# Kernel tuning notes

Measured on AMD Instinct MI355X. Metric: run time of the kernel, lower is better.

## Reference

```python
import jax, jax.numpy as jnp
import numpy as np
import math

D_MODEL = 768
H = 12
D_K = D_MODEL // H


def setup_inputs() -> dict:
    key = jax.random.key(0)
    ks = jax.random.split(key, 12)
    B, S = 2, 2048
    q = jax.random.normal(ks[0], (B, S, D_MODEL), dtype=jnp.float32)
    k = jax.random.normal(ks[1], (B, S, D_MODEL), dtype=jnp.float32)
    v = jax.random.normal(ks[2], (B, S, D_MODEL), dtype=jnp.float32)
    mask = jax.random.randint(ks[3], (1, 1, S, S), 0, 2, dtype=jnp.int32)
    scale = 1.0 / math.sqrt(D_MODEL)
    w_q = jax.random.normal(ks[4], (D_MODEL, D_MODEL), dtype=jnp.float32) * scale
    b_q = jnp.zeros((D_MODEL,), dtype=jnp.float32)
    w_k = jax.random.normal(ks[5], (D_MODEL, D_MODEL), dtype=jnp.float32) * scale
    b_k = jnp.zeros((D_MODEL,), dtype=jnp.float32)
    w_v = jax.random.normal(ks[6], (D_MODEL, D_MODEL), dtype=jnp.float32) * scale
    b_v = jnp.zeros((D_MODEL,), dtype=jnp.float32)
    w_o = jax.random.normal(ks[7], (D_MODEL, D_MODEL), dtype=jnp.float32) * scale
    b_o = jnp.zeros((D_MODEL,), dtype=jnp.float32)
    return {"q": q, "k": k, "v": v, "mask": mask,
            "w_q": w_q, "b_q": b_q, "w_k": w_k, "b_k": b_k,
            "w_v": w_v, "b_v": b_v, "w_o": w_o, "b_o": b_o}


def reference(q, k, v, mask, w_q, b_q, w_k, b_k, w_v, b_v, w_o, b_o):
    B, S, _ = q.shape
    # torch nn.Linear: y = x @ W^T + b
    qp = (q @ w_q.T + b_q).reshape(B, S, H, D_K).transpose(0, 2, 1, 3)  # [B,H,S,Dk]
    kp = (k @ w_k.T + b_k).reshape(B, S, H, D_K).transpose(0, 2, 1, 3)
    vp = (v @ w_v.T + b_v).reshape(B, S, H, D_K).transpose(0, 2, 1, 3)
    # full [B,H,S,S] score matrix (the memory-bound round-trip)
    scores = jnp.einsum('bhqd,bhkd->bhqk', qp, kp) / math.sqrt(D_K)
    scores = jnp.where(mask == 0, jnp.float32(-1e9), scores)
    attn = jax.nn.softmax(scores, axis=-1)
    x = jnp.einsum('bhqk,bhkd->bhqd', attn, vp)  # [B,H,S,Dk]
    x = x.transpose(0, 2, 1, 3).reshape(B, S, H * D_K)
    return x @ w_o.T + b_o
```

## Files before the change

kernel.cpp:

```cpp
#include <hip/hip_runtime.h>
#include <hip/hip_bf16.h>

typedef __attribute__((ext_vector_type(8))) __bf16 bf16x8;
typedef __attribute__((ext_vector_type(8))) short short8;
typedef __attribute__((ext_vector_type(4))) float f32x4;

#define LOG2E 1.44269504088896f
#define SCL (0.125f * 1.44269504088896f)

static __device__ __forceinline__ ushort f2bf(float f) {
  union { float f; unsigned u; } x; x.f = f;
  unsigned r = x.u + 0x7fffu + ((x.u >> 16) & 1u);
  return (ushort)(r >> 16);
}

static __device__ __forceinline__ unsigned cvt_pk_bf16(float a, float b) {
  unsigned r;
  asm("v_cvt_pk_bf16_f32 %0, %1, %2" : "=v"(r) : "v"(a), "v"(b));
  return r;
}

static __device__ __forceinline__ void gll16(const ushort* g, ushort* l) {
  __builtin_amdgcn_global_load_lds(
      (const __attribute__((address_space(1))) unsigned*)g,
      (__attribute__((address_space(3))) unsigned*)l, 16, 0, 0);
}

#define NQ 3145728u
#define NW 589824u
__global__ __launch_bounds__(256)
void cvt_all(const float* __restrict__ q, const float* __restrict__ k,
             const float* __restrict__ v,
             const float* __restrict__ wq, const float* __restrict__ wk,
             const float* __restrict__ wv, const float* __restrict__ wo,
             ushort* __restrict__ dst)
{
  size_t i = ((size_t)blockIdx.x * 256 + threadIdx.x) * 4;
  const float* src; size_t off;
  if (i < NQ)            { src = q; off = i; }
  else if (i < 2u * NQ)  { src = k; off = i - NQ; }
  else if (i < 3u * NQ)  { src = v; off = i - 2u * NQ; }
  else {
    size_t j = i - 3u * NQ;
    unsigned wsel = (unsigned)(j / NW);
    off = j % NW;
    src = (wsel == 0) ? wq : (wsel == 1) ? wk : (wsel == 2) ? wv : wo;
  }
  f32x4 x = *(const f32x4*)(src + off);
  uint2 o;
  o.x = cvt_pk_bf16(x[0], x[1]);
  o.y = cvt_pk_bf16(x[2], x[3]);
  *(uint2*)(dst + i) = o;
}

__global__ __launch_bounds__(256)
void mask_pack(const int* __restrict__ mask, unsigned long long* __restrict__ mb)
{
  size_t gw = (size_t)blockIdx.x * 4 + (threadIdx.x >> 6);
  int lane = threadIdx.x & 63;
  int mk = mask[gw * 64 + lane];
  unsigned long long bits = __ballot(mk != 0);
  if (lane == 0) mb[gw] = bits;
}

template<int MODE>
static __device__ __forceinline__ void gemm_core(const ushort* __restrict__ A,
                                                 const ushort* __restrict__ Wrow0,
                                                 const float* __restrict__ bias0,
                                                 void* __restrict__ outv,
                                                 int m0, int c0)
{
  constexpr int K = 768;
  __shared__ ushort As[128 * 32];
  __shared__ ushort Bs[128 * 32];
  const int tid  = threadIdx.x;
  const int lane = tid & 63;
  const int wid  = tid >> 6;
  const int wr = (wid >> 1) * 64;
  const int wc = (wid & 1) * 64;

  f32x4 acc[4][4];
#pragma unroll
  for (int i = 0; i < 4; i++)
#pragma unroll
    for (int j = 0; j < 4; j++) acc[i][j] = f32x4{0.f, 0.f, 0.f, 0.f};

  const int srow = wid * 16 + (lane >> 2);
  const int scol = (lane & 3) * 8;
  const ushort* gA0 = A     + (size_t)(m0 + srow) * K + scol;
  const ushort* gA1 = gA0 + (size_t)64 * K;
  const ushort* gB0 = Wrow0 + (size_t)srow * K + scol;
  const ushort* gB1 = gB0 + (size_t)64 * K;
  ushort* lA0 = &As[srow * 32 + scol];
  ushort* lA1 = &As[(srow + 64) * 32 + scol];
  ushort* lB0 = &Bs[srow * 32 + scol];
  ushort* lB1 = &Bs[(srow + 64) * 32 + scol];

  const int fr  = lane & 15;
  const int kg8 = (lane >> 4) * 8;

  for (int kt = 0; kt < K; kt += 32) {
    __syncthreads();
    gll16(gA0 + kt, lA0);
    gll16(gA1 + kt, lA1);
    gll16(gB0 + kt, lB0);
    gll16(gB1 + kt, lB1);
    __syncthreads();

    bf16x8 af[4], wf[4];
#pragma unroll
    for (int i = 0; i < 4; i++) af[i] = *(const bf16x8*)&As[(wr + i * 16 + fr) * 32 + kg8];
#pragma unroll
    for (int j = 0; j < 4; j++) wf[j] = *(const bf16x8*)&Bs[(wc + j * 16 + fr) * 32 + kg8];
#pragma unroll
    for (int i = 0; i < 4; i++)
#pragma unroll
      for (int j = 0; j < 4; j++)
        acc[i][j] = __builtin_amdgcn_mfma_f32_16x16x32_bf16(af[i], wf[j], acc[i][j], 0, 0, 0);
  }

#pragma unroll
  for (int i = 0; i < 4; i++) {
#pragma unroll
    for (int j = 0; j < 4; j++) {
#pragma unroll
      for (int r = 0; r < 4; r++) {
        int m  = m0 + wr + i * 16 + (lane >> 4) * 4 + r;
        int lc = wc + j * 16 + fr;
        float val = acc[i][j][r] + bias0[lc];
        if (MODE == 0) {
          int nn = c0 + lc;
          int hh = nn >> 6, dk = nn & 63;
          ((ushort*)outv)[(((size_t)(m >> 11) * 12 + hh) * 2048 + (m & 2047)) * 64 + dk] = f2bf(val);
        } else {
          ((float*)outv)[(size_t)m * 768 + c0 + lc] = val;
        }
      }
    }
  }
}

__global__ __launch_bounds__(256)
void qkv_gemm2(const ushort* __restrict__ CV,
               const float* __restrict__ bq, const float* __restrict__ bk,
               const float* __restrict__ bv,
               ushort* __restrict__ Qp, ushort* __restrict__ Kp, ushort* __restrict__ Vp)
{
  const int m0 = blockIdx.x * 128;
  const int n0 = blockIdx.y * 128;
  const int proj = n0 / 768;
  const int c0 = n0 - proj * 768;
  const ushort* A  = CV + (size_t)proj * NQ;
  const ushort* Wc = CV + (size_t)3 * NQ;
  const float* bias = (proj == 0) ? bq : (proj == 1) ? bk : bv;
  ushort* O = (proj == 0) ? Qp : (proj == 1) ? Kp : Vp;
  gemm_core<0>(A, Wc + (size_t)n0 * 768, bias + c0, O, m0, c0);
}

__global__ __launch_bounds__(256)
void o_gemm2(const ushort* __restrict__ X, const ushort* __restrict__ Wo,
             const float* __restrict__ bo, float* __restrict__ out)
{
  const int m0 = blockIdx.x * 128;
  const int n0 = blockIdx.y * 128;
  gemm_core<1>(X, Wo + (size_t)n0 * 768, bo + n0, out, m0, n0);
}

__global__ __launch_bounds__(256, 3)
void attn_kernel(const ushort* __restrict__ Qp, const ushort* __restrict__ Kp,
                 const ushort* __restrict__ Vp,
                 const unsigned long long* __restrict__ mb,
                 ushort* __restrict__ X)
{
  constexpr int S = 2048;
  __shared__ ushort Ks[128][72];
  __shared__ ushort Vt[64][136];
  __shared__ ushort Ps[4][16][136];

  const int tid  = threadIdx.x;
  const int lane = tid & 63;
  const int w    = tid >> 6;
  const int bid  = blockIdx.x;
  const int bh = (bid & 7) + 8 * (bid >> 8);
  const int qb = (bid >> 3) & 31;
  const int b = bh / 12, h = bh % 12;

  const ushort* Qb = Qp + (size_t)bh * S * 64;
  const ushort* Kb = Kp + (size_t)bh * S * 64;
  const ushort* Vb = Vp + (size_t)bh * S * 64;

  const int q0  = qb * 64;
  const int fr  = lane & 15;
  const int g   = lane >> 4;
  const int kg8 = g * 8;
  const int qrow4 = q0 + w * 16 + g * 4;

  const int qrow = q0 + w * 16 + fr;
  bf16x8 qf0 = *(const bf16x8*)&Qb[(size_t)qrow * 64 + kg8];
  bf16x8 qf1 = *(const bf16x8*)&Qb[(size_t)qrow * 64 + 32 + kg8];

  float m_r[4] = {-1e9f, -1e9f, -1e9f, -1e9f};
  float l_r[4] = {0.f, 0.f, 0.f, 0.f};
  f32x4 accO[4];
#pragma unroll
  for (int ni = 0; ni < 4; ni++) accO[ni] = f32x4{0.f, 0.f, 0.f, 0.f};

  const int skey = tid >> 2;
  const int sc0  = (tid & 3) * 16;
  const uint4* mb4 = (const uint4*)mb;

  short8 kr0, kr1, kr2, kr3, vr0, vr1, vr2, vr3;
  {
    const ushort* kb = Kb + (size_t)skey * 64 + sc0;
    const ushort* vb = Vb + (size_t)skey * 64 + sc0;
    kr0 = *(const short8*)kb;          kr1 = *(const short8*)(kb + 8);
    kr2 = *(const short8*)(kb + 4096); kr3 = *(const short8*)(kb + 4104);
    vr0 = *(const short8*)vb;          vr1 = *(const short8*)(vb + 8);
    vr2 = *(const short8*)(vb + 4096); vr3 = *(const short8*)(vb + 4104);
  }

  for (int tt = 0; tt < 16; tt++) {
    __syncthreads();
    *(short8*)&Ks[skey][sc0]          = kr0;
    *(short8*)&Ks[skey][sc0 + 8]      = kr1;
    *(short8*)&Ks[64 + skey][sc0]     = kr2;
    *(short8*)&Ks[64 + skey][sc0 + 8] = kr3;
#pragma unroll
    for (int i = 0; i < 8; i++) {
      Vt[sc0 + i][skey]          = (ushort)vr0[i];
      Vt[sc0 + 8 + i][skey]      = (ushort)vr1[i];
      Vt[sc0 + i][64 + skey]     = (ushort)vr2[i];
      Vt[sc0 + 8 + i][64 + skey] = (ushort)vr3[i];
    }
    __syncthreads();

    uint4 mB[4];
#pragma unroll
    for (int r = 0; r < 4; r++)
      mB[r] = mb4[(size_t)(qrow4 + r) * 16 + tt];

    if (tt < 15) {
      const ushort* kb = Kb + (size_t)((tt + 1) * 128 + skey) * 64 + sc0;
      const ushort* vb = Vb + (size_t)((tt + 1) * 128 + skey) * 64 + sc0;
      kr0 = *(const short8*)kb;          kr1 = *(const short8*)(kb + 8);
      kr2 = *(const short8*)(kb + 4096); kr3 = *(const short8*)(kb + 4104);
      vr0 = *(const short8*)vb;          vr1 = *(const short8*)(vb + 8);
      vr2 = *(const short8*)(vb + 4096); vr3 = *(const short8*)(vb + 4104);
    }

    f32x4 sc8[8];
#pragma unroll
    for (int ni = 0; ni < 8; ni++) {
      bf16x8 kf0 = *(const bf16x8*)&Ks[ni * 16 + fr][kg8];
      bf16x8 kf1 = *(const bf16x8*)&Ks[ni * 16 + fr][32 + kg8];
      f32x4 c = {0.f, 0.f, 0.f, 0.f};
      c = __builtin_amdgcn_mfma_f32_16x16x32_bf16(qf0, kf0, c, 0, 0, 0);
      c = __builtin_amdgcn_mfma_f32_16x16x32_bf16(qf1, kf1, c, 0, 0, 0);
      sc8[ni] = c;
    }

#pragma unroll
    for (int r = 0; r < 4; r++) {
      float praw[8];
#pragma unroll
      for (int ni = 0; ni < 8; ni++) praw[ni] = sc8[ni][r] * SCL;
      float mx = fmaxf(fmaxf(fmaxf(praw[0], praw[1]), fmaxf(praw[2], praw[3])),
                       fmaxf(fmaxf(praw[4], praw[5]), fmaxf(praw[6], praw[7])));
      mx = fmaxf(mx, __shfl_xor(mx, 1));
      mx = fmaxf(mx, __shfl_xor(mx, 2));
      mx = fmaxf(mx, __shfl_xor(mx, 4));
      mx = fmaxf(mx, __shfl_xor(mx, 8));
      if (mx > m_r[r] + 11.5f) {
        float al = exp2f(m_r[r] - mx);
        m_r[r] = mx;
        l_r[r] *= al;
#pragma unroll
        for (int ni = 0; ni < 4; ni++) accO[ni][r] *= al;
      }
      const float mr = m_r[r];
      unsigned sx = mB[r].x >> fr, sy = mB[r].y >> fr,
               sz = mB[r].z >> fr, sw = mB[r].w >> fr;
      unsigned bits[8] = { sx & 1u, (sx >> 16) & 1u, sy & 1u, (sy >> 16) & 1u,
                           sz & 1u, (sz >> 16) & 1u, sw & 1u, (sw >> 16) & 1u };
      float e[8];
      float ls = 0.f;
#pragma unroll
      for (int ni = 0; ni < 8; ni++) {
        float t = exp2f(praw[ni] - mr);
        t = bits[ni] ? t : 0.f;
        e[ni] = t; ls += t;
      }
      ls += __shfl_xor(ls, 1);
      ls += __shfl_xor(ls, 2);
      ls += __shfl_xor(ls, 4);
      ls += __shfl_xor(ls, 8);
      l_r[r] += ls;
#pragma unroll
      for (int a = 0; a < 4; a++) {
        unsigned pk = cvt_pk_bf16(e[2 * a], e[2 * a + 1]);
        Ps[w][g * 4 + r][a * 32 + fr]      = (ushort)pk;
        Ps[w][g * 4 + r][a * 32 + 16 + fr] = (ushort)(pk >> 16);
      }
    }

#pragma unroll
    for (int ks = 0; ks < 4; ks++) {
      bf16x8 pf = *(const bf16x8*)&Ps[w][fr][ks * 32 + kg8];
#pragma unroll
      for (int ni = 0; ni < 4; ni++) {
        bf16x8 vf = *(const bf16x8*)&Vt[ni * 16 + fr][ks * 32 + kg8];
        accO[ni] = __builtin_amdgcn_mfma_f32_16x16x32_bf16(pf, vf, accO[ni], 0, 0, 0);
      }
    }
  }

  float inv[4];
#pragma unroll
  for (int r = 0; r < 4; r++) inv[r] = 1.f / l_r[r];
#pragma unroll
  for (int ni = 0; ni < 4; ni++) {
#pragma unroll
    for (int r = 0; r < 4; r++) {
      int qq = qrow4 + r;
      float o = accO[ni][r] * inv[r];
      X[((size_t)b * S + qq) * 768 + h * 64 + ni * 16 + fr] = f2bf(o);
    }
  }
}

extern "C" void kernel_launch(void* const* d_in, const int* in_sizes, int n_in,
                              void* d_out, int out_size, void* d_ws, size_t ws_size,
                              hipStream_t stream) {
  const float* q  = (const float*)d_in[0];
  const float* k  = (const float*)d_in[1];
  const float* v  = (const float*)d_in[2];
  const int* mask = (const int*)d_in[3];
  const float* wq = (const float*)d_in[4];
  const float* bq = (const float*)d_in[5];
  const float* wk = (const float*)d_in[6];
  const float* bk = (const float*)d_in[7];
  const float* wv = (const float*)d_in[8];
  const float* bv = (const float*)d_in[9];
  const float* wo = (const float*)d_in[10];
  const float* bo = (const float*)d_in[11];
  float* out = (float*)d_out;

  ushort* CV = (ushort*)d_ws;
  ushort* Qp = CV + (size_t)3 * NQ + (size_t)4 * NW;
  ushort* Kp = Qp + NQ;
  ushort* Vp = Kp + NQ;
  ushort* Xb = Vp + NQ;
  unsigned long long* mbuf = (unsigned long long*)CV;

  cvt_all<<<11520, 256, 0, stream>>>(q, k, v, wq, wk, wv, wo, CV);
  qkv_gemm2<<<dim3(32, 18), dim3(256), 0, stream>>>(CV, bq, bk, bv, Qp, Kp, Vp);
  mask_pack<<<16384, 256, 0, stream>>>(mask, mbuf);
  attn_kernel<<<768, 256, 0, stream>>>(Qp, Kp, Vp, mbuf, Xb);
  o_gemm2<<<dim3(32, 6), dim3(256), 0, stream>>>(Xb, CV + (size_t)3 * NQ + (size_t)3 * NW, bo, out);
}
```

Before: 264.1 us.

## Double-buffer GEMM LDS tiles with BK=64 and prefetch next tile

Restructures the projection GEMM main loop to use two LDS buffers with a K-tile of 64. The next tile's global-to-LDS loads are issued before computing on the current one, and each iteration now needs one barrier instead of two. The cvt kernel's per-thread division and modulo for weight selection is replaced with compare chains. LDS use grows to 64KB per block, which may lower occupancy, and the prefetch relies on the barrier-implied wait for the async LDS loads to finish.

```diff
diff --git a/kernel.cpp b/kernel.cpp
--- a/kernel.cpp
+++ b/kernel.cpp
@@ -37,14 +37,15 @@
 {
   size_t i = ((size_t)blockIdx.x * 256 + threadIdx.x) * 4;
   const float* src; size_t off;
-  if (i < NQ)            { src = q; off = i; }
-  else if (i < 2u * NQ)  { src = k; off = i - NQ; }
-  else if (i < 3u * NQ)  { src = v; off = i - 2u * NQ; }
+  if (i < NQ)                { src = q;  off = i; }
+  else if (i < 2u * NQ)      { src = k;  off = i - NQ; }
+  else if (i < 3u * NQ)      { src = v;  off = i - 2u * NQ; }
   else {
     size_t j = i - 3u * NQ;
-    unsigned wsel = (unsigned)(j / NW);
-    off = j % NW;
-    src = (wsel == 0) ? wq : (wsel == 1) ? wk : (wsel == 2) ? wv : wo;
+    if (j < NW)            { src = wq; off = j; }
+    else if (j < 2u * NW)  { src = wk; off = j - NW; }
+    else if (j < 3u * NW)  { src = wv; off = j - 2u * NW; }
+    else                   { src = wo; off = j - 3u * NW; }
   }
   f32x4 x = *(const f32x4*)(src + off);
   uint2 o;
@@ -71,8 +72,9 @@
                                                  int m0, int c0)
 {
   constexpr int K = 768;
-  __shared__ ushort As[128 * 32];
-  __shared__ ushort Bs[128 * 32];
+  constexpr int BK = 64;
+  __shared__ ushort As[2][128 * BK];
+  __shared__ ushort Bs[2][128 * BK];
   const int tid  = threadIdx.x;
   const int lane = tid & 63;
   const int wid  = tid >> 6;
@@ -85,38 +87,54 @@
 #pragma unroll
     for (int j = 0; j < 4; j++) acc[i][j] = f32x4{0.f, 0.f, 0.f, 0.f};
 
-  const int srow = wid * 16 + (lane >> 2);
-  const int scol = (lane & 3) * 8;
-  const ushort* gA0 = A     + (size_t)(m0 + srow) * K + scol;
-  const ushort* gA1 = gA0 + (size_t)64 * K;
-  const ushort* gB0 = Wrow0 + (size_t)srow * K + scol;
-  const ushort* gB1 = gB0 + (size_t)64 * K;
-  ushort* lA0 = &As[srow * 32 + scol];
-  ushort* lA1 = &As[(srow + 64) * 32 + scol];
-  ushort* lB0 = &Bs[srow * 32 + scol];
-  ushort* lB1 = &Bs[(srow + 64) * 32 + scol];
+  const ushort* gA[4]; const ushort* gB[4];
+  int loff[4];
+#pragma unroll
+  for (int s = 0; s < 4; s++) {
+    int idx = tid + s * 256;
+    int row = idx >> 3, col = (idx & 7) * 8;
+    gA[s] = A     + (size_t)(m0 + row) * K + col;
+    gB[s] = Wrow0 + (size_t)row * K + col;
+    loff[s] = idx * 8;
+  }
 
   const int fr  = lane & 15;
   const int kg8 = (lane >> 4) * 8;
 
-  for (int kt = 0; kt < K; kt += 32) {
+#pragma unroll
+  for (int s = 0; s < 4; s++) {
+    gll16(gA[s], &As[0][loff[s]]);
+    gll16(gB[s], &Bs[0][loff[s]]);
+  }
+  __syncthreads();
+
+  int cur = 0;
+  for (int t = 0; t < K / BK; t++) {
+    if (t < K / BK - 1) {
+      const int kt = (t + 1) * BK;
+#pragma unroll
+      for (int s = 0; s < 4; s++) {
+        gll16(gA[s] + kt, &As[cur ^ 1][loff[s]]);
+        gll16(gB[s] + kt, &Bs[cur ^ 1][loff[s]]);
+      }
+    }
+    bf16x8 af[2][4], wf[2][4];
+#pragma unroll
+    for (int kk = 0; kk < 2; kk++) {
+#pragma unroll
+      for (int i = 0; i < 4; i++) af[kk][i] = *(const bf16x8*)&As[cur][(wr + i * 16 + fr) * BK + kk * 32 + kg8];
+#pragma unroll
+      for (int j = 0; j < 4; j++) wf[kk][j] = *(const bf16x8*)&Bs[cur][(wc + j * 16 + fr) * BK + kk * 32 + kg8];
+    }
+#pragma unroll
+    for (int kk = 0; kk < 2; kk++)
+#pragma unroll
+      for (int i = 0; i < 4; i++)
+#pragma unroll
+        for (int j = 0; j < 4; j++)
+          acc[i][j] = __builtin_amdgcn_mfma_f32_16x16x32_bf16(af[kk][i], wf[kk][j], acc[i][j], 0, 0, 0);
     __syncthreads();
-    gll16(gA0 + kt, lA0);
-    gll16(gA1 + kt, lA1);
-    gll16(gB0 + kt, lB0);
-    gll16(gB1 + kt, lB1);
-    __syncthreads();
-
-    bf16x8 af[4], wf[4];
-#pragma unroll
-    for (int i = 0; i < 4; i++) af[i] = *(const bf16x8*)&As[(wr + i * 16 + fr) * 32 + kg8];
-#pragma unroll
-    for (int j = 0; j < 4; j++) wf[j] = *(const bf16x8*)&Bs[(wc + j * 16 + fr) * 32 + kg8];
-#pragma unroll
-    for (int i = 0; i < 4; i++)
-#pragma unroll
-      for (int j = 0; j < 4; j++)
-        acc[i][j] = __builtin_amdgcn_mfma_f32_16x16x32_bf16(af[i], wf[j], acc[i][j], 0, 0, 0);
+    cur ^= 1;
   }
 
 #pragma unroll
```

After: 266.1 us. No clear change (+0.8%).
